# Optimization experiments

Measured on AMD Instinct MI355X. Metric: run time of the kernel, lower is better.

Reference implementation:

```python
import jax, jax.numpy as jnp
import numpy as np

N_HEADS = 16
D_EMBED = 1024
SEQ = 1024  # must equal D_EMBED: GroupNorm is applied on dim1 of (b, seq, c)
BATCH = 4
GROUPS = 32
EPS = 1e-6


def setup_inputs() -> dict:
    key = jax.random.key(0)
    ks = jax.random.split(key, 7)
    c = D_EMBED
    s = 0.02
    return {
        "x": jax.random.normal(ks[0], (BATCH, SEQ, c), dtype=jnp.float32),
        "gn_w": jnp.ones((SEQ,), dtype=jnp.float32),  # GroupNorm affine over dim1 (= seq here)
        "gn_b": jnp.zeros((SEQ,), dtype=jnp.float32),
        "w_qkv": jax.random.normal(ks[1], (3 * c, c), dtype=jnp.float32) * s,
        "b_qkv": jnp.zeros((3 * c,), dtype=jnp.float32),
        "w_out": jax.random.normal(ks[2], (c, c), dtype=jnp.float32) * s,
        "b_out": jnp.zeros((c,), dtype=jnp.float32),
    }


def _group_norm_dim1(x, w, b):
    # Faithful to torch.nn.GroupNorm applied to (B, S, C): dim1 (S) is the
    # channel dim; normalize over each group of S//GROUPS rows together with C.
    bsz, s, c = x.shape
    xg = x.reshape(bsz, GROUPS, (s // GROUPS) * c)
    mu = jnp.mean(xg, axis=-1, keepdims=True)
    var = jnp.var(xg, axis=-1, keepdims=True)
    xn = ((xg - mu) * jax.lax.rsqrt(var + EPS)).reshape(bsz, s, c)
    return xn * w[None, :, None] + b[None, :, None]


def reference(x, gn_w, gn_b, w_qkv, b_qkv, w_out, b_out):
    bsz, seq, c = x.shape
    dh = c // N_HEADS
    h = _group_norm_dim1(x, gn_w, gn_b)
    qkv = h @ w_qkv.T + b_qkv  # (b, s, 3c)
    q, k, v = jnp.split(qkv, 3, axis=-1)
    # (b, s, H, dh) -> (b, H, s, dh)
    q = q.reshape(bsz, seq, N_HEADS, dh).transpose(0, 2, 1, 3)
    k = k.reshape(bsz, seq, N_HEADS, dh).transpose(0, 2, 1, 3)
    v = v.reshape(bsz, seq, N_HEADS, dh).transpose(0, 2, 1, 3)
    # NOTE: source divides by sqrt(d_head) TWICE -> effective scale 1/d_head
    w = jnp.einsum("bhqd,bhkd->bhqk", q, k) / float(dh)
    w = jax.nn.softmax(w, axis=-1)
    o = jnp.einsum("bhqk,bhkd->bhqd", w, v)  # (b, H, s, dh)
    # NOTE: source calls .transpose(1,2) without assignment, then .view(b,s,c):
    # faithful behavior is a raw reshape of the (b, H, s, dh) tensor.
    o = o.reshape(bsz, seq, c)
    o = o @ w_out.T + b_out
    return x + o
```

## Files before the change

kernel.cpp:

```cpp
#include <hip/hip_runtime.h>

typedef __bf16 bf16_t;
typedef bf16_t bf16x8 __attribute__((ext_vector_type(8)));
typedef bf16_t bf16x4 __attribute__((ext_vector_type(4)));
typedef float f32x4 __attribute__((ext_vector_type(4)));

__device__ __forceinline__ void gload_lds16(const bf16_t* g, bf16_t* l) {
    __builtin_amdgcn_global_load_lds(
        (const __attribute__((address_space(1))) void*)g,
        (__attribute__((address_space(3))) void*)l, 16, 0, 0);
}

__global__ __launch_bounds__(256, 2) void prep_kernel(const float* __restrict__ x,
        const float* __restrict__ gw, const float* __restrict__ gb, bf16_t* __restrict__ h,
        const float* __restrict__ in1, const float* __restrict__ in2,
        bf16_t* __restrict__ out1, bf16_t* __restrict__ out2, int n1_4, int ntot_4) {
    if (blockIdx.x >= 128) {
        int i = (blockIdx.x - 128) * 256 + threadIdx.x;
        if (i < ntot_4) {
            const float* in = (i < n1_4) ? in1 : in2;
            bf16_t* out = (i < n1_4) ? out1 : out2;
            int j = (i < n1_4) ? i : i - n1_4;
            float4 v = reinterpret_cast<const float4*>(in)[j];
            bf16x4 o;
            o[0] = (bf16_t)v.x; o[1] = (bf16_t)v.y; o[2] = (bf16_t)v.z; o[3] = (bf16_t)v.w;
            *reinterpret_cast<bf16x4*>(out + (size_t)j * 4) = o;
        }
        return;
    }
    int bg = blockIdx.x;
    int batch = bg >> 5, g = bg & 31;
    const float* xp = x + ((size_t)batch * 1024 + g * 32) * 1024;
    float4 xr[32];
    float s = 0.f, s2 = 0.f;
    #pragma unroll
    for (int i = 0; i < 32; ++i) {
        float4 v = reinterpret_cast<const float4*>(xp)[threadIdx.x + i * 256];
        xr[i] = v;
        s  += v.x + v.y + v.z + v.w;
        s2 += v.x*v.x + v.y*v.y + v.z*v.z + v.w*v.w;
    }
    #pragma unroll
    for (int o = 32; o >= 1; o >>= 1) {
        s  += __shfl_down(s, o, 64);
        s2 += __shfl_down(s2, o, 64);
    }
    __shared__ float ps[4], ps2[4];
    __shared__ float stat[2];
    if ((threadIdx.x & 63) == 0) { ps[threadIdx.x >> 6] = s; ps2[threadIdx.x >> 6] = s2; }
    __syncthreads();
    if (threadIdx.x == 0) {
        float S  = ps[0] + ps[1] + ps[2] + ps[3];
        float S2 = ps2[0] + ps2[1] + ps2[2] + ps2[3];
        float mu  = S * (1.f / 32768.f);
        float var = S2 * (1.f / 32768.f) - mu * mu;
        stat[0] = mu; stat[1] = rsqrtf(var + 1e-6f);
    }
    __syncthreads();
    float mu = stat[0], rs = stat[1];
    bf16_t* hp = h + ((size_t)batch * 1024 + g * 32) * 1024;
    #pragma unroll
    for (int i = 0; i < 32; ++i) {
        int idx = threadIdx.x + i * 256;
        int row = idx >> 8;
        float a = rs * gw[g * 32 + row];
        float b = gb[g * 32 + row] - mu * a;
        float4 v = xr[i];
        bf16x4 o;
        o[0] = (bf16_t)(v.x * a + b); o[1] = (bf16_t)(v.y * a + b);
        o[2] = (bf16_t)(v.z * a + b); o[3] = (bf16_t)(v.w * a + b);
        *reinterpret_cast<bf16x4*>(hp + (size_t)idx * 4) = o;
    }
}

__global__ __launch_bounds__(512, 2) void gemm256_kernel(
        const bf16_t* __restrict__ A, const bf16_t* __restrict__ W,
        const float* __restrict__ bias, bf16_t* __restrict__ outp,
        int M, int N, int K) {
    __shared__ bf16_t As[2][2][128 * 64];
    __shared__ bf16_t Bs[2][3][64 * 64];
    int cpx = gridDim.x >> 3;
    int bid = blockIdx.x;
    int tile = (bid & 7) * cpx + (bid >> 3);
    int bx = tile & 15, by = tile >> 4;
    int m0 = by * 256, n0 = bx * 192;
    int t = threadIdx.x, l = t & 63, wid = t >> 6;
    int lr = l & 15, lg = l >> 4;
    int gm = (wid >> 2) * 128 + ((wid >> 1) & 1) * 64;
    int gn = (wid & 1) * 96;
    int ah = wid >> 2;
    int aml = ((wid >> 1) & 1) * 64;

    int c0 = t, c1 = t + 512;
    int r0 = c0 >> 3, col0 = (((c0 & 7) ^ (r0 & 7)) << 3);
    int r1 = c1 >> 3, col1 = (((c1 & 7) ^ (r1 & 7)) << 3);

    f32x4 acc[4][6] = {};

#define STAGE_A(slot, hf, kt) { \
        const bf16_t* _s = A + (size_t)(m0 + (hf) * 128) * K + (kt) * 64; \
        gload_lds16(_s + (size_t)r0 * K + col0, &As[slot][hf][c0 * 8]); \
        gload_lds16(_s + (size_t)r1 * K + col1, &As[slot][hf][c1 * 8]); }
#define STAGE_B3(slot, th, kt) { \
        const bf16_t* _s = W + (size_t)(n0 + (th) * 64) * K + (kt) * 64; \
        gload_lds16(_s + (size_t)r0 * K + col0, &Bs[slot][th][c0 * 8]); }
#define LOAD_AF(slot, mq) \
        _Pragma("unroll") \
        for (int i = 0; i < 2; ++i) { \
            int row = aml + (mq) * 32 + i * 16 + lr; \
            _Pragma("unroll") \
            for (int kk = 0; kk < 2; ++kk) \
                afr[i][kk] = *reinterpret_cast<const bf16x8*>( \
                    &As[slot][ah][row * 64 + (((kk * 4 + lg) ^ (row & 7)) << 3)]); }
#define LOAD_BF(slot, dst, nq) \
        _Pragma("unroll") \
        for (int j = 0; j < 3; ++j) { \
            int col = gn + (nq) * 48 + j * 16 + lr; \
            _Pragma("unroll") \
            for (int kk = 0; kk < 2; ++kk) \
                dst[j][kk] = *reinterpret_cast<const bf16x8*>( \
                    &Bs[slot][col >> 6][(col & 63) * 64 + (((kk * 4 + lg) ^ (col & 7)) << 3)]); }
#define MFMA_Q(mq, nq, bfr) \
        __builtin_amdgcn_s_setprio(1); \
        _Pragma("unroll") \
        for (int i = 0; i < 2; ++i) \
            _Pragma("unroll") \
            for (int j = 0; j < 3; ++j) \
                _Pragma("unroll") \
                for (int kk = 0; kk < 2; ++kk) \
                    acc[(mq) * 2 + i][(nq) * 3 + j] = __builtin_amdgcn_mfma_f32_16x16x32_bf16( \
                        afr[i][kk], bfr[j][kk], acc[(mq) * 2 + i][(nq) * 3 + j], 0, 0, 0); \
        __builtin_amdgcn_s_setprio(0);

    STAGE_A(0, 0, 0) STAGE_B3(0, 0, 0) STAGE_B3(0, 1, 0) STAGE_B3(0, 2, 0) STAGE_A(0, 1, 0)
    asm volatile("s_waitcnt vmcnt(0)" ::: "memory");
    __builtin_amdgcn_s_barrier();

    const int NT = K >> 6;
    for (int kt = 0; kt < NT - 1; ++kt) {
        int cur = kt & 1, nxt = cur ^ 1;
        bf16x8 afr[2][2], bf0[3][2], bf1[3][2];
        LOAD_AF(cur, 0) LOAD_BF(cur, bf0, 0)
        STAGE_A(nxt, 0, kt + 1)
        __builtin_amdgcn_s_barrier();
        MFMA_Q(0, 0, bf0)
        asm volatile("s_waitcnt vmcnt(4)" ::: "memory");
        __builtin_amdgcn_s_barrier();
        LOAD_BF(cur, bf1, 1)
        STAGE_B3(nxt, 0, kt + 1)
        STAGE_B3(nxt, 1, kt + 1)
        __builtin_amdgcn_s_barrier();
        MFMA_Q(0, 1, bf1)
        asm volatile("s_waitcnt vmcnt(4)" ::: "memory");
        __builtin_amdgcn_s_barrier();
        LOAD_AF(cur, 1)
        STAGE_B3(nxt, 2, kt + 1)
        __builtin_amdgcn_s_barrier();
        MFMA_Q(1, 1, bf1)
        __builtin_amdgcn_s_barrier();
        STAGE_A(nxt, 1, kt + 1)
        __builtin_amdgcn_s_barrier();
        MFMA_Q(1, 0, bf0)
        asm volatile("s_waitcnt vmcnt(4)" ::: "memory");
        __builtin_amdgcn_s_barrier();
    }
    {
        int cur = (NT - 1) & 1;
        asm volatile("s_waitcnt vmcnt(0)" ::: "memory");
        __builtin_amdgcn_s_barrier();
        bf16x8 afr[2][2], bf0[3][2], bf1[3][2];
        LOAD_AF(cur, 0) LOAD_BF(cur, bf0, 0) LOAD_BF(cur, bf1, 1)
        MFMA_Q(0, 0, bf0)
        MFMA_Q(0, 1, bf1)
        LOAD_AF(cur, 1)
        MFMA_Q(1, 1, bf1)
        MFMA_Q(1, 0, bf0)
    }

    #pragma unroll
    for (int mf = 0; mf < 4; ++mf) {
        #pragma unroll
        for (int r = 0; r < 4; ++r) {
            int row = m0 + gm + mf * 16 + lg * 4 + r;
            #pragma unroll
            for (int nf = 0; nf < 6; ++nf) {
                int col = n0 + gn + nf * 16 + lr;
                outp[(size_t)row * N + col] = (bf16_t)(acc[mf][nf][r] + bias[col]);
            }
        }
    }
#undef STAGE_A
#undef STAGE_B3
#undef LOAD_AF
#undef LOAD_BF
#undef MFMA_Q
}

template <int EPI, int BM>
__global__ __launch_bounds__(256) void gemm_nt_kernel(
        const bf16_t* __restrict__ A, const bf16_t* __restrict__ W,
        const float* __restrict__ bias, void* __restrict__ outp,
        const float* __restrict__ resid, int M, int N, int K, int lda) {
    constexpr int MF = BM / 32;
    __shared__ bf16_t As[BM * 64];
    __shared__ bf16_t Bs[128 * 64];
    int nbx = N >> 7;
    int cpx = gridDim.x >> 3;
    int bid = blockIdx.x;
    int tile = (bid & 7) * cpx + (bid >> 3);
    int bx = tile % nbx, by = tile / nbx;
    int m0 = by * BM, n0 = bx * 128;
    int t = threadIdx.x, l = t & 63, wid = t >> 6;
    int wm = (wid >> 1) * (BM / 2), wn = (wid & 1) * 64;
    int lr = l & 15, lg = l >> 4;

    f32x4 acc[MF][4] = {};
    for (int k0 = 0; k0 < K; k0 += 64) {
        #pragma unroll
        for (int i = 0; i < BM / 32; ++i) {
            int c = t + i * 256;
            int row = c >> 3, cc = c & 7;
            int col = (cc ^ (row & 7)) << 3;
            gload_lds16(A + (size_t)(m0 + row) * lda + k0 + col, &As[c * 8]);
        }
        #pragma unroll
        for (int i = 0; i < 4; ++i) {
            int c = t + i * 256;
            int row = c >> 3, cc = c & 7;
            int col = (cc ^ (row & 7)) << 3;
            gload_lds16(W + (size_t)(n0 + row) * K + k0 + col, &Bs[c * 8]);
        }
        __syncthreads();
        #pragma unroll
        for (int s = 0; s < 2; ++s) {
            int xo = ((s * 4 + lg) ^ (lr & 7)) << 3;
            bf16x8 af[MF], bfr[4];
            #pragma unroll
            for (int mf = 0; mf < MF; ++mf)
                af[mf] = *reinterpret_cast<const bf16x8*>(&As[(wm + mf * 16 + lr) * 64 + xo]);
            #pragma unroll
            for (int nf = 0; nf < 4; ++nf)
                bfr[nf] = *reinterpret_cast<const bf16x8*>(&Bs[(wn + nf * 16 + lr) * 64 + xo]);
            #pragma unroll
            for (int mf = 0; mf < MF; ++mf) {
                #pragma unroll
                for (int nf = 0; nf < 4; ++nf)
                    acc[mf][nf] = __builtin_amdgcn_mfma_f32_16x16x32_bf16(af[mf], bfr[nf], acc[mf][nf], 0, 0, 0);
            }
        }
        __syncthreads();
    }
    #pragma unroll
    for (int mf = 0; mf < MF; ++mf) {
        #pragma unroll
        for (int r = 0; r < 4; ++r) {
            int row = m0 + wm + mf * 16 + lg * 4 + r;
            #pragma unroll
            for (int nf = 0; nf < 4; ++nf) {
                int col = n0 + wn + nf * 16 + lr;
                float v = acc[mf][nf][r] + bias[col];
                if (EPI == 0) {
                    reinterpret_cast<bf16_t*>(outp)[(size_t)row * N + col] = (bf16_t)v;
                } else {
                    size_t idx = (size_t)row * N + col;
                    reinterpret_cast<float*>(outp)[idx] = v + resid[idx];
                }
            }
        }
    }
}

__global__ __launch_bounds__(256) void frag_prep_kernel(const bf16_t* __restrict__ qkv,
                                                        bf16_t* __restrict__ kfrag,
                                                        bf16_t* __restrict__ vfrag) {
    __shared__ bf16_t ktile[32 * 72];
    __shared__ bf16_t vt[32 * 72];
    int t = threadIdx.x;
    int kt = blockIdx.x & 31, bh = blockIdx.x >> 5;
    int b = bh >> 4, hh = bh & 15;
    const bf16_t* kbase = qkv + ((size_t)b * 1024 + kt * 32) * 3072 + 1024 + hh * 64;
    const bf16_t* vbase = kbase + 1024;
    {
        int row = t >> 3, c = t & 7;
        bf16x8 kv = *reinterpret_cast<const bf16x8*>(kbase + (size_t)row * 3072 + c * 8);
        *reinterpret_cast<bf16x8*>(&ktile[row * 72 + c * 8]) = kv;
        bf16x8 vv = *reinterpret_cast<const bf16x8*>(vbase + (size_t)row * 3072 + c * 8);
        *reinterpret_cast<bf16x8*>(&vt[row * 72 + c * 8]) = vv;
    }
    __syncthreads();
    {
        int f = (t >> 7) & 1, m = (t >> 6) & 1, l = t & 63;
        bf16x8 v = *reinterpret_cast<const bf16x8*>(
            &ktile[(f * 16 + (l & 15)) * 72 + m * 32 + ((l >> 4) & 3) * 8]);
        *reinterpret_cast<bf16x8*>(kfrag + ((size_t)bh * 32 + kt) * 2048 + t * 8) = v;
    }
    {
        int nf = (t >> 6) & 3, l = t & 63;
        int d = nf * 16 + (l & 15);
        int lg = (l >> 4) & 3;
        bf16x8 o;
        #pragma unroll
        for (int j = 0; j < 8; ++j) {
            int kpos = lg * 8 + j;
            int kl = ((kpos & 4) << 2) | ((kpos & 24) >> 1) | (kpos & 3);
            o[j] = vt[kl * 72 + d];
        }
        *reinterpret_cast<bf16x8*>(vfrag + ((size_t)bh * 32 + kt) * 2048 + t * 8) = o;
    }
}

__global__ __launch_bounds__(256, 2) void attn_kernel(const bf16_t* __restrict__ qkv,
                                                      const bf16_t* __restrict__ kfrag,
                                                      const bf16_t* __restrict__ vfrag,
                                                      bf16_t* __restrict__ oq) {
    int bid = blockIdx.x;
    int tile = (bid & 7) * 64 + (bid >> 3);
    int qt = tile & 7, bh = tile >> 3;
    int hh = bh & 15, bb = bh >> 4;
    int t = threadIdx.x, l = t & 63, wid = t >> 6;
    int lr = l & 15, lg = (l >> 4) & 3;

    bf16x8 qf[2][2];
    #pragma unroll
    for (int s = 0; s < 2; ++s) {
        int qrow = qt * 128 + wid * 32 + s * 16 + lr;
        const bf16_t* qp = qkv + ((size_t)bb * 1024 + qrow) * 3072 + hh * 64;
        bf16x8 q0 = *reinterpret_cast<const bf16x8*>(qp + lg * 8);
        bf16x8 q1 = *reinterpret_cast<const bf16x8*>(qp + 32 + lg * 8);
        #pragma unroll
        for (int j = 0; j < 8; ++j) {
            qf[s][0][j] = (bf16_t)((float)q0[j] * 0.02254211001f);
            qf[s][1][j] = (bf16_t)((float)q1[j] * 0.02254211001f);
        }
    }

    const bf16_t* kfb = kfrag + (size_t)bh * 65536 + l * 8;
    const bf16_t* vfb = vfrag + (size_t)bh * 65536 + l * 8;

    f32x4 acc[2][4] = {};
    float den0 = 0.f, den1 = 0.f;

    bf16x8 kA[4], vA[4], kB[4], vB[4];

#define LOADSET(kS, vS, tt) { \
        const bf16_t* _k = kfb + (tt) * 2048; \
        const bf16_t* _v = vfb + (tt) * 2048; \
        kS[0] = *reinterpret_cast<const bf16x8*>(_k); \
        kS[1] = *reinterpret_cast<const bf16x8*>(_k + 512); \
        kS[2] = *reinterpret_cast<const bf16x8*>(_k + 1024); \
        kS[3] = *reinterpret_cast<const bf16x8*>(_k + 1536); \
        vS[0] = *reinterpret_cast<const bf16x8*>(_v); \
        vS[1] = *reinterpret_cast<const bf16x8*>(_v + 512); \
        vS[2] = *reinterpret_cast<const bf16x8*>(_v + 1024); \
        vS[3] = *reinterpret_cast<const bf16x8*>(_v + 1536); }

#define EX(x) __builtin_amdgcn_exp2f(x)

#define COMPUTE(kS, vS) { \
        f32x4 z00 = {0.f,0.f,0.f,0.f}, z01 = {0.f,0.f,0.f,0.f}; \
        f32x4 z10 = {0.f,0.f,0.f,0.f}, z11 = {0.f,0.f,0.f,0.f}; \
        z00 = __builtin_amdgcn_mfma_f32_16x16x32_bf16(kS[0], qf[0][0], z00, 0, 0, 0); \
        z10 = __builtin_amdgcn_mfma_f32_16x16x32_bf16(kS[0], qf[1][0], z10, 0, 0, 0); \
        z01 = __builtin_amdgcn_mfma_f32_16x16x32_bf16(kS[2], qf[0][0], z01, 0, 0, 0); \
        z11 = __builtin_amdgcn_mfma_f32_16x16x32_bf16(kS[2], qf[1][0], z11, 0, 0, 0); \
        z00 = __builtin_amdgcn_mfma_f32_16x16x32_bf16(kS[1], qf[0][1], z00, 0, 0, 0); \
        z10 = __builtin_amdgcn_mfma_f32_16x16x32_bf16(kS[1], qf[1][1], z10, 0, 0, 0); \
        z01 = __builtin_amdgcn_mfma_f32_16x16x32_bf16(kS[3], qf[0][1], z01, 0, 0, 0); \
        z11 = __builtin_amdgcn_mfma_f32_16x16x32_bf16(kS[3], qf[1][1], z11, 0, 0, 0); \
        float a0 = EX(z00[0]), a1 = EX(z00[1]), a2 = EX(z00[2]), a3 = EX(z00[3]); \
        float a4 = EX(z01[0]), a5 = EX(z01[1]), a6 = EX(z01[2]), a7 = EX(z01[3]); \
        float b0 = EX(z10[0]), b1 = EX(z10[1]), b2 = EX(z10[2]), b3 = EX(z10[3]); \
        float b4 = EX(z11[0]), b5 = EX(z11[1]), b6 = EX(z11[2]), b7 = EX(z11[3]); \
        den0 += ((a0 + a1) + (a2 + a3)) + ((a4 + a5) + (a6 + a7)); \
        den1 += ((b0 + b1) + (b2 + b3)) + ((b4 + b5) + (b6 + b7)); \
        bf16x8 pa0, pa1; \
        pa0[0] = (bf16_t)a0; pa0[1] = (bf16_t)a1; pa0[2] = (bf16_t)a2; pa0[3] = (bf16_t)a3; \
        pa0[4] = (bf16_t)a4; pa0[5] = (bf16_t)a5; pa0[6] = (bf16_t)a6; pa0[7] = (bf16_t)a7; \
        pa1[0] = (bf16_t)b0; pa1[1] = (bf16_t)b1; pa1[2] = (bf16_t)b2; pa1[3] = (bf16_t)b3; \
        pa1[4] = (bf16_t)b4; pa1[5] = (bf16_t)b5; pa1[6] = (bf16_t)b6; pa1[7] = (bf16_t)b7; \
        acc[0][0] = __builtin_amdgcn_mfma_f32_16x16x32_bf16(pa0, vS[0], acc[0][0], 0, 0, 0); \
        acc[0][1] = __builtin_amdgcn_mfma_f32_16x16x32_bf16(pa0, vS[1], acc[0][1], 0, 0, 0); \
        acc[0][2] = __builtin_amdgcn_mfma_f32_16x16x32_bf16(pa0, vS[2], acc[0][2], 0, 0, 0); \
        acc[0][3] = __builtin_amdgcn_mfma_f32_16x16x32_bf16(pa0, vS[3], acc[0][3], 0, 0, 0); \
        acc[1][0] = __builtin_amdgcn_mfma_f32_16x16x32_bf16(pa1, vS[0], acc[1][0], 0, 0, 0); \
        acc[1][1] = __builtin_amdgcn_mfma_f32_16x16x32_bf16(pa1, vS[1], acc[1][1], 0, 0, 0); \
        acc[1][2] = __builtin_amdgcn_mfma_f32_16x16x32_bf16(pa1, vS[2], acc[1][2], 0, 0, 0); \
        acc[1][3] = __builtin_amdgcn_mfma_f32_16x16x32_bf16(pa1, vS[3], acc[1][3], 0, 0, 0); }

    LOADSET(kA, vA, 0)
    for (int kt = 0; kt < 32; kt += 2) {
        __builtin_amdgcn_s_barrier();
        LOADSET(kB, vB, kt + 1)
        COMPUTE(kA, vA)
        if (kt + 2 < 32) LOADSET(kA, vA, kt + 2)
        COMPUTE(kB, vB)
    }
#undef LOADSET
#undef COMPUTE
#undef EX

    float rs0[4], rs1[4];
    {
        float v0 = den0, v1 = den1;
        v0 += __shfl_xor(v0, 16, 64);
        v0 += __shfl_xor(v0, 32, 64);
        v1 += __shfl_xor(v1, 16, 64);
        v1 += __shfl_xor(v1, 32, 64);
        #pragma unroll
        for (int r = 0; r < 4; ++r) {
            rs0[r] = 1.f / __shfl(v0, (l & 48) | (lg * 4 + r), 64);
            rs1[r] = 1.f / __shfl(v1, (l & 48) | (lg * 4 + r), 64);
        }
    }

    size_t obase = ((size_t)bh * 1024 + qt * 128 + wid * 32) * 64;
    #pragma unroll
    for (int s = 0; s < 2; ++s) {
        #pragma unroll
        for (int nf = 0; nf < 4; ++nf) {
            #pragma unroll
            for (int r = 0; r < 4; ++r) {
                int q = s * 16 + lg * 4 + r;
                int d = nf * 16 + lr;
                size_t flat = obase + (size_t)q * 64 + d;
                float dn = s == 0 ? rs0[r] : rs1[r];
                oq[(flat >> 10) * 3072 + 1024 + (flat & 1023)] =
                    (bf16_t)(acc[s][nf][r] * dn);
            }
        }
    }
}

extern "C" void kernel_launch(void* const* d_in, const int* in_sizes, int n_in,
                              void* d_out, int out_size, void* d_ws, size_t ws_size,
                              hipStream_t stream) {
    const float* x     = (const float*)d_in[0];
    const float* gn_w  = (const float*)d_in[1];
    const float* gn_b  = (const float*)d_in[2];
    const float* w_qkv = (const float*)d_in[3];
    const float* b_qkv = (const float*)d_in[4];
    const float* w_out = (const float*)d_in[5];
    const float* b_out = (const float*)d_in[6];
    float* out = (float*)d_out;

    bf16_t* h      = (bf16_t*)d_ws;
    bf16_t* wqkv_b = h + (size_t)4096 * 1024;
    bf16_t* wout_b = wqkv_b + (size_t)3072 * 1024;
    bf16_t* qkvb   = wout_b + (size_t)1024 * 1024;
    bf16_t* kfrag  = qkvb + (size_t)4096 * 3072;
    bf16_t* vfrag  = h;

    const int n1_4 = 3072 * 1024 / 4, ntot_4 = n1_4 + 1024 * 1024 / 4;
    prep_kernel<<<128 + (ntot_4 + 255) / 256, 256, 0, stream>>>(
        x, gn_w, gn_b, h, w_qkv, w_out, wqkv_b, wout_b, n1_4, ntot_4);
    gemm256_kernel<<<256, 512, 0, stream>>>(h, wqkv_b, b_qkv, qkvb, 4096, 3072, 1024);
    frag_prep_kernel<<<2048, 256, 0, stream>>>(qkvb, kfrag, vfrag);
    attn_kernel<<<512, 256, 0, stream>>>(qkvb, kfrag, vfrag, qkvb);
    gemm_nt_kernel<1, 64><<<512, 256, 0, stream>>>(qkvb + 1024, wout_b, b_out, (void*)out, x,
                                                   4096, 1024, 1024, 3072);
}
```

Before: 92.65 us.

## Stage K fragments through double-buffered LDS shared by all waves

In the attention kernel, each wave used to load its own copy of every K tile from global memory into registers. Now the block cooperatively loads each K tile once into a double-buffered shared-memory array using direct global-to-LDS loads, and the waves read their fragments from LDS. V is still loaded straight from global memory. This cuts redundant global and L2 traffic for K, but it adds a full vmcnt(0) wait and a barrier on every iteration and drops the old two-tile register prefetch of V, which may expose load latency.

```diff
diff --git a/kernel.cpp b/kernel.cpp
--- a/kernel.cpp
+++ b/kernel.cpp
@@ -313,6 +313,7 @@
                                                       const bf16_t* __restrict__ kfrag,
                                                       const bf16_t* __restrict__ vfrag,
                                                       bf16_t* __restrict__ oq) {
+    __shared__ bf16_t Kl[2][2048];
     int bid = blockIdx.x;
     int tile = (bid & 7) * 64 + (bid >> 3);
     int qt = tile & 7, bh = tile >> 3;
@@ -334,69 +335,67 @@
         }
     }
 
-    const bf16_t* kfb = kfrag + (size_t)bh * 65536 + l * 8;
-    const bf16_t* vfb = vfrag + (size_t)bh * 65536 + l * 8;
+    const bf16_t* ksrc = kfrag + (size_t)bh * 65536;
+    const bf16_t* vfb  = vfrag + (size_t)bh * 65536 + l * 8;
 
     f32x4 acc[2][4] = {};
     float den0 = 0.f, den1 = 0.f;
 
-    bf16x8 kA[4], vA[4], kB[4], vB[4];
-
-#define LOADSET(kS, vS, tt) { \
-        const bf16_t* _k = kfb + (tt) * 2048; \
-        const bf16_t* _v = vfb + (tt) * 2048; \
-        kS[0] = *reinterpret_cast<const bf16x8*>(_k); \
-        kS[1] = *reinterpret_cast<const bf16x8*>(_k + 512); \
-        kS[2] = *reinterpret_cast<const bf16x8*>(_k + 1024); \
-        kS[3] = *reinterpret_cast<const bf16x8*>(_k + 1536); \
-        vS[0] = *reinterpret_cast<const bf16x8*>(_v); \
-        vS[1] = *reinterpret_cast<const bf16x8*>(_v + 512); \
-        vS[2] = *reinterpret_cast<const bf16x8*>(_v + 1024); \
-        vS[3] = *reinterpret_cast<const bf16x8*>(_v + 1536); }
-
 #define EX(x) __builtin_amdgcn_exp2f(x)
 
-#define COMPUTE(kS, vS) { \
-        f32x4 z00 = {0.f,0.f,0.f,0.f}, z01 = {0.f,0.f,0.f,0.f}; \
-        f32x4 z10 = {0.f,0.f,0.f,0.f}, z11 = {0.f,0.f,0.f,0.f}; \
-        z00 = __builtin_amdgcn_mfma_f32_16x16x32_bf16(kS[0], qf[0][0], z00, 0, 0, 0); \
-        z10 = __builtin_amdgcn_mfma_f32_16x16x32_bf16(kS[0], qf[1][0], z10, 0, 0, 0); \
-        z01 = __builtin_amdgcn_mfma_f32_16x16x32_bf16(kS[2], qf[0][0], z01, 0, 0, 0); \
-        z11 = __builtin_amdgcn_mfma_f32_16x16x32_bf16(kS[2], qf[1][0], z11, 0, 0, 0); \
-        z00 = __builtin_amdgcn_mfma_f32_16x16x32_bf16(kS[1], qf[0][1], z00, 0, 0, 0); \
-        z10 = __builtin_amdgcn_mfma_f32_16x16x32_bf16(kS[1], qf[1][1], z10, 0, 0, 0); \
-        z01 = __builtin_amdgcn_mfma_f32_16x16x32_bf16(kS[3], qf[0][1], z01, 0, 0, 0); \
-        z11 = __builtin_amdgcn_mfma_f32_16x16x32_bf16(kS[3], qf[1][1], z11, 0, 0, 0); \
-        float a0 = EX(z00[0]), a1 = EX(z00[1]), a2 = EX(z00[2]), a3 = EX(z00[3]); \
-        float a4 = EX(z01[0]), a5 = EX(z01[1]), a6 = EX(z01[2]), a7 = EX(z01[3]); \
-        float b0 = EX(z10[0]), b1 = EX(z10[1]), b2 = EX(z10[2]), b3 = EX(z10[3]); \
-        float b4 = EX(z11[0]), b5 = EX(z11[1]), b6 = EX(z11[2]), b7 = EX(z11[3]); \
-        den0 += ((a0 + a1) + (a2 + a3)) + ((a4 + a5) + (a6 + a7)); \
-        den1 += ((b0 + b1) + (b2 + b3)) + ((b4 + b5) + (b6 + b7)); \
-        bf16x8 pa0, pa1; \
-        pa0[0] = (bf16_t)a0; pa0[1] = (bf16_t)a1; pa0[2] = (bf16_t)a2; pa0[3] = (bf16_t)a3; \
-        pa0[4] = (bf16_t)a4; pa0[5] = (bf16_t)a5; pa0[6] = (bf16_t)a6; pa0[7] = (bf16_t)a7; \
-        pa1[0] = (bf16_t)b0; pa1[1] = (bf16_t)b1; pa1[2] = (bf16_t)b2; pa1[3] = (bf16_t)b3; \
-        pa1[4] = (bf16_t)b4; pa1[5] = (bf16_t)b5; pa1[6] = (bf16_t)b6; pa1[7] = (bf16_t)b7; \
-        acc[0][0] = __builtin_amdgcn_mfma_f32_16x16x32_bf16(pa0, vS[0], acc[0][0], 0, 0, 0); \
-        acc[0][1] = __builtin_amdgcn_mfma_f32_16x16x32_bf16(pa0, vS[1], acc[0][1], 0, 0, 0); \
-        acc[0][2] = __builtin_amdgcn_mfma_f32_16x16x32_bf16(pa0, vS[2], acc[0][2], 0, 0, 0); \
-        acc[0][3] = __builtin_amdgcn_mfma_f32_16x16x32_bf16(pa0, vS[3], acc[0][3], 0, 0, 0); \
-        acc[1][0] = __builtin_amdgcn_mfma_f32_16x16x32_bf16(pa1, vS[0], acc[1][0], 0, 0, 0); \
-        acc[1][1] = __builtin_amdgcn_mfma_f32_16x16x32_bf16(pa1, vS[1], acc[1][1], 0, 0, 0); \
-        acc[1][2] = __builtin_amdgcn_mfma_f32_16x16x32_bf16(pa1, vS[2], acc[1][2], 0, 0, 0); \
-        acc[1][3] = __builtin_amdgcn_mfma_f32_16x16x32_bf16(pa1, vS[3], acc[1][3], 0, 0, 0); }
-
-    LOADSET(kA, vA, 0)
-    for (int kt = 0; kt < 32; kt += 2) {
-        __builtin_amdgcn_s_barrier();
-        LOADSET(kB, vB, kt + 1)
-        COMPUTE(kA, vA)
-        if (kt + 2 < 32) LOADSET(kA, vA, kt + 2)
-        COMPUTE(kB, vB)
-    }
-#undef LOADSET
-#undef COMPUTE
+    gload_lds16(ksrc + t * 8, &Kl[0][t * 8]);
+    asm volatile("s_waitcnt vmcnt(0)" ::: "memory");
+    __builtin_amdgcn_s_barrier();
+
+    for (int kt = 0; kt < 32; ++kt) {
+        int cur = kt & 1, nxt = cur ^ 1;
+        bf16x8 vS[4];
+        const bf16_t* _v = vfb + kt * 2048;
+        vS[0] = *reinterpret_cast<const bf16x8*>(_v);
+        vS[1] = *reinterpret_cast<const bf16x8*>(_v + 512);
+        vS[2] = *reinterpret_cast<const bf16x8*>(_v + 1024);
+        vS[3] = *reinterpret_cast<const bf16x8*>(_v + 1536);
+        if (kt < 31)
+            gload_lds16(ksrc + (kt + 1) * 2048 + t * 8, &Kl[nxt][t * 8]);
+        bf16x8 kS[4];
+        kS[0] = *reinterpret_cast<const bf16x8*>(&Kl[cur][l * 8]);
+        kS[1] = *reinterpret_cast<const bf16x8*>(&Kl[cur][512 + l * 8]);
+        kS[2] = *reinterpret_cast<const bf16x8*>(&Kl[cur][1024 + l * 8]);
+        kS[3] = *reinterpret_cast<const bf16x8*>(&Kl[cur][1536 + l * 8]);
+
+        f32x4 z00 = {0.f,0.f,0.f,0.f}, z01 = {0.f,0.f,0.f,0.f};
+        f32x4 z10 = {0.f,0.f,0.f,0.f}, z11 = {0.f,0.f,0.f,0.f};
+        z00 = __builtin_amdgcn_mfma_f32_16x16x32_bf16(kS[0], qf[0][0], z00, 0, 0, 0);
+        z10 = __builtin_amdgcn_mfma_f32_16x16x32_bf16(kS[0], qf[1][0], z10, 0, 0, 0);
+        z01 = __builtin_amdgcn_mfma_f32_16x16x32_bf16(kS[2], qf[0][0], z01, 0, 0, 0);
+        z11 = __builtin_amdgcn_mfma_f32_16x16x32_bf16(kS[2], qf[1][0], z11, 0, 0, 0);
+        z00 = __builtin_amdgcn_mfma_f32_16x16x32_bf16(kS[1], qf[0][1], z00, 0, 0, 0);
+        z10 = __builtin_amdgcn_mfma_f32_16x16x32_bf16(kS[1], qf[1][1], z10, 0, 0, 0);
+        z01 = __builtin_amdgcn_mfma_f32_16x16x32_bf16(kS[3], qf[0][1], z01, 0, 0, 0);
+        z11 = __builtin_amdgcn_mfma_f32_16x16x32_bf16(kS[3], qf[1][1], z11, 0, 0, 0);
+        float a0 = EX(z00[0]), a1 = EX(z00[1]), a2 = EX(z00[2]), a3 = EX(z00[3]);
+        float a4 = EX(z01[0]), a5 = EX(z01[1]), a6 = EX(z01[2]), a7 = EX(z01[3]);
+        float b0 = EX(z10[0]), b1 = EX(z10[1]), b2 = EX(z10[2]), b3 = EX(z10[3]);
+        float b4 = EX(z11[0]), b5 = EX(z11[1]), b6 = EX(z11[2]), b7 = EX(z11[3]);
+        den0 += ((a0 + a1) + (a2 + a3)) + ((a4 + a5) + (a6 + a7));
+        den1 += ((b0 + b1) + (b2 + b3)) + ((b4 + b5) + (b6 + b7));
+        bf16x8 pa0, pa1;
+        pa0[0] = (bf16_t)a0; pa0[1] = (bf16_t)a1; pa0[2] = (bf16_t)a2; pa0[3] = (bf16_t)a3;
+        pa0[4] = (bf16_t)a4; pa0[5] = (bf16_t)a5; pa0[6] = (bf16_t)a6; pa0[7] = (bf16_t)a7;
+        pa1[0] = (bf16_t)b0; pa1[1] = (bf16_t)b1; pa1[2] = (bf16_t)b2; pa1[3] = (bf16_t)b3;
+        pa1[4] = (bf16_t)b4; pa1[5] = (bf16_t)b5; pa1[6] = (bf16_t)b6; pa1[7] = (bf16_t)b7;
+        acc[0][0] = __builtin_amdgcn_mfma_f32_16x16x32_bf16(pa0, vS[0], acc[0][0], 0, 0, 0);
+        acc[0][1] = __builtin_amdgcn_mfma_f32_16x16x32_bf16(pa0, vS[1], acc[0][1], 0, 0, 0);
+        acc[0][2] = __builtin_amdgcn_mfma_f32_16x16x32_bf16(pa0, vS[2], acc[0][2], 0, 0, 0);
+        acc[0][3] = __builtin_amdgcn_mfma_f32_16x16x32_bf16(pa0, vS[3], acc[0][3], 0, 0, 0);
+        acc[1][0] = __builtin_amdgcn_mfma_f32_16x16x32_bf16(pa1, vS[0], acc[1][0], 0, 0, 0);
+        acc[1][1] = __builtin_amdgcn_mfma_f32_16x16x32_bf16(pa1, vS[1], acc[1][1], 0, 0, 0);
+        acc[1][2] = __builtin_amdgcn_mfma_f32_16x16x32_bf16(pa1, vS[2], acc[1][2], 0, 0, 0);
+        acc[1][3] = __builtin_amdgcn_mfma_f32_16x16x32_bf16(pa1, vS[3], acc[1][3], 0, 0, 0);
+
+        asm volatile("s_waitcnt vmcnt(0)" ::: "memory");
+        __builtin_amdgcn_s_barrier();
+    }
 #undef EX
 
     float rs0[4], rs1[4];
```

After: 95.34 us. +2.9%, slower.
